# Kernel tuning notes

Measured on AMD Instinct MI355X. Metric: run time of the kernel, lower is better.

The kernel has to match this reference:

```python
import jax, jax.numpy as jnp
import numpy as np
from jax import lax

SCALE = 2
K_UP = 5
EPS = 1e-5
DN = ('NCHW', 'OIHW', 'NCHW')


def _bn(x, gamma, beta, mean, var):
    inv = gamma / jnp.sqrt(var + EPS)
    return x * inv[None, :, None, None] + (beta - mean * inv)[None, :, None, None]


def _pixel_shuffle(x, r):
    b, crr, h, w = x.shape
    c = crr // (r * r)
    x = x.reshape(b, c, r, r, h, w)
    x = x.transpose(0, 1, 4, 2, 5, 3)  # b, c, h, r, w, r
    return x.reshape(b, c, h * r, w * r)


def setup_inputs() -> dict:
    key = jax.random.key(0)
    ks = jax.random.split(key, 4)
    b, c, h, w = 4, 64, 128, 128
    c_mid = 64
    enc_out = (SCALE * K_UP) ** 2  # 100
    return {
        'X': jax.random.normal(ks[0], (b, c, h, w), jnp.float32),
        'comp_w': jax.random.normal(ks[1], (c_mid, c, 1, 1), jnp.float32) * 0.1,
        'comp_gamma': jnp.ones((c_mid,), jnp.float32),
        'comp_beta': jnp.zeros((c_mid,), jnp.float32),
        'comp_mean': jnp.zeros((c_mid,), jnp.float32),
        'comp_var': jnp.ones((c_mid,), jnp.float32),
        'enc_w': jax.random.normal(ks[2], (enc_out, c_mid, 3, 3), jnp.float32) * 0.05,
        'enc_b': jnp.zeros((enc_out,), jnp.float32),
        'enc_gamma': jnp.ones((enc_out,), jnp.float32),
        'enc_beta': jnp.zeros((enc_out,), jnp.float32),
        'enc_mean': jnp.zeros((enc_out,), jnp.float32),
        'enc_var': jnp.ones((enc_out,), jnp.float32),
    }


def reference(X, comp_w, comp_gamma, comp_beta, comp_mean, comp_var,
              enc_w, enc_b, enc_gamma, enc_beta, enc_mean, enc_var):
    b, c, h, w = X.shape
    h_, w_ = h * SCALE, w * SCALE
    # compress: 1x1 conv + BN + ReLU
    Wm = lax.conv_general_dilated(X, comp_w, (1, 1), 'VALID', dimension_numbers=DN)
    Wm = jax.nn.relu(_bn(Wm, comp_gamma, comp_beta, comp_mean, comp_var))
    # encode kernel weights: 3x3 conv + BN
    Wm = lax.conv_general_dilated(Wm, enc_w, (1, 1), ((1, 1), (1, 1)), dimension_numbers=DN)
    Wm = Wm + enc_b[None, :, None, None]
    Wm = _bn(Wm, enc_gamma, enc_beta, enc_mean, enc_var)
    # pixel shuffle -> [b, k_up^2, h_, w_], softmax over kernel dim
    Wm = _pixel_shuffle(Wm, SCALE)
    Wm = jax.nn.softmax(Wm, axis=1)
    # nearest upsample input
    Xu = jnp.repeat(jnp.repeat(X, SCALE, axis=2), SCALE, axis=3)  # [b,c,h_,w_]
    # unfold(k=5, dilation=2, pad=4) + einsum, fused as accumulation over the
    # 25 kernel taps (avoids the b*c*25*h_*w_ im2col blowup; identical math)
    pad = (K_UP // 2) * SCALE  # 4
    Xp = jnp.pad(Xu, ((0, 0), (0, 0), (pad, pad), (pad, pad)))
    out = jnp.zeros((b, c, h_, w_), X.dtype)
    for i in range(K_UP):
        for j in range(K_UP):
            k = i * K_UP + j
            patch = lax.dynamic_slice(Xp, (0, 0, i * SCALE, j * SCALE), (b, c, h_, w_))
            out = out + Wm[:, k:k + 1] * patch
    return out
```

## Files before the change

kernel.cpp:

```cpp
#include <hip/hip_runtime.h>

#define EPS 1e-5f

typedef __attribute__((ext_vector_type(8))) short short8;
typedef __attribute__((ext_vector_type(4))) float float4v;

__device__ inline unsigned short f2bf(float f) {
  unsigned u = __float_as_uint(f);
  unsigned r = (u + 0x7fffu + ((u >> 16) & 1u)) >> 16;
  return (unsigned short)r;
}
__device__ inline uint pk2(float a, float b) {
  return (uint)f2bf(a) | ((uint)f2bf(b) << 16);
}

__global__ __launch_bounds__(256) void xform_kernel(
    const float* __restrict__ enc_w, const float* __restrict__ enc_gamma,
    const float* __restrict__ enc_var, const float* __restrict__ comp_w,
    const float* __restrict__ comp_gamma, const float* __restrict__ comp_var,
    const float* __restrict__ enc_b, const float* __restrict__ enc_beta,
    const float* __restrict__ enc_mean, const float* __restrict__ comp_beta,
    const float* __restrict__ comp_mean, ushort* __restrict__ Awt,
    float* __restrict__ Wc, float* __restrict__ bias2,
    float* __restrict__ bias_c) {
  int u = blockIdx.x * 256 + threadIdx.x;
  if (u < 9216) {
    int kc = u >> 9, rem = u & 511;
    int mt = rem >> 6, q = (rem >> 4) & 3, ml = rem & 15;
    int e = mt * 16 + ml;
    int t = kc >> 1, h = kc & 1;
    int dy = t / 3, dx = t - dy * 3;
    float inv = (e < 100) ? enc_gamma[e] * rsqrtf(enc_var[e] + EPS) : 0.f;
    ushort o[8];
#pragma unroll
    for (int j = 0; j < 8; ++j) {
      int ci = h * 32 + q * 8 + j;
      float w = (e < 100) ? enc_w[(e * 64 + ci) * 9 + dy * 3 + dx] * inv : 0.f;
      o[j] = f2bf(w);
    }
    uint4 v;
    v.x = (uint)o[0] | ((uint)o[1] << 16);
    v.y = (uint)o[2] | ((uint)o[3] << 16);
    v.z = (uint)o[4] | ((uint)o[5] << 16);
    v.w = (uint)o[6] | ((uint)o[7] << 16);
    *reinterpret_cast<uint4*>(Awt + (size_t)u * 8) = v;
  } else if (u < 13312) {
    int v = u - 9216;
    int co = v & 63;
    float inv = comp_gamma[co] * rsqrtf(comp_var[co] + EPS);
    Wc[v] = comp_w[co * 64 + (v >> 6)] * inv;
  } else if (u < 13440) {
    int t = u - 13312;
    float v = 0.f;
    if (t < 100) {
      float inv = enc_gamma[t] * rsqrtf(enc_var[t] + EPS);
      v = enc_b[t] * inv + enc_beta[t] - enc_mean[t] * inv;
    }
    bias2[t] = v;
  } else if (u < 13504) {
    int c = u - 13440;
    float inv = comp_gamma[c] * rsqrtf(comp_var[c] + EPS);
    bias_c[c] = comp_beta[c] - comp_mean[c] * inv;
  }
}

__global__ __launch_bounds__(256) void compress_kernel(
    const float* __restrict__ X, const float* __restrict__ Wc,
    const float* __restrict__ bias_c, ushort* __restrict__ out,
    ushort* __restrict__ Xb) {
  __shared__ __align__(16) float xtile[64 * 65];
  __shared__ __align__(16) float osm[64 * 68];
  const int tid = threadIdx.x;
  const int p0 = blockIdx.x * 64;
  const int b = p0 >> 14;
  const float* xbase = X + ((size_t)b << 20) + (p0 & 16383);

#pragma unroll
  for (int k = 0; k < 16; ++k) {
    int u = k * 256 + tid;
    int ci = u >> 6, px = u & 63;
    xtile[px * 65 + ci] = xbase[((size_t)ci << 14) + px];
  }
  __syncthreads();

  const int wv = __builtin_amdgcn_readfirstlane(tid >> 6);
  const int ln = tid & 63;
  float acc[16];
#pragma unroll
  for (int u = 0; u < 16; ++u) acc[u] = bias_c[wv * 16 + u];
  const float* xr = xtile + ln * 65;
#pragma unroll 8
  for (int ci = 0; ci < 64; ++ci) {
    float xv = xr[ci];
    const float* wr = Wc + ci * 64 + wv * 16;
#pragma unroll
    for (int u = 0; u < 16; ++u) acc[u] = fmaf(wr[u], xv, acc[u]);
  }
  float4v* orow = reinterpret_cast<float4v*>(osm) + ln * 17 + wv * 4;
#pragma unroll
  for (int j = 0; j < 4; ++j) {
    float4v t;
#pragma unroll
    for (int s = 0; s < 4; ++s) t[s] = fmaxf(acc[j * 4 + s], 0.f);
    orow[j] = t;
  }
  __syncthreads();

#pragma unroll
  for (int j = 0; j < 2; ++j) {
    int u = j * 256 + tid;
    int px = u >> 3, g = u & 7;
    const float* so = osm + px * 68 + g * 8;
    uint4 vo = make_uint4(pk2(so[0], so[1]), pk2(so[2], so[3]),
                          pk2(so[4], so[5]), pk2(so[6], so[7]));
    *reinterpret_cast<uint4*>(out + (size_t)(p0 + px) * 64 + g * 8) = vo;
    const float* sx = xtile + px * 65 + g * 8;
    uint4 vx = make_uint4(pk2(sx[0], sx[1]), pk2(sx[2], sx[3]),
                          pk2(sx[4], sx[5]), pk2(sx[6], sx[7]));
    *reinterpret_cast<uint4*>(Xb + (size_t)(p0 + px) * 64 + g * 8) = vx;
  }
}

__global__ __launch_bounds__(256) void encode_mfma(
    const ushort* __restrict__ Wm1t, const ushort* __restrict__ Awt,
    const float* __restrict__ bias2, uint* __restrict__ Wtu) {
  __shared__ __align__(16) char smem[25856];
  ushort* Xt = (ushort*)smem;
  const int tid = threadIdx.x;
  const int b = blockIdx.z;
  const int y0 = blockIdx.y * 8, x0 = blockIdx.x * 8;

  for (int u = tid; u < 800; u += 256) {
    int pos = u >> 3, cg = u & 7;
    int iy = pos / 10, ix = pos - iy * 10;
    int gy = y0 + iy - 1, gx = x0 + ix - 1;
    uint4 v = make_uint4(0, 0, 0, 0);
    if ((unsigned)gy < 128u && (unsigned)gx < 128u)
      v = *reinterpret_cast<const uint4*>(
          Wm1t + ((((size_t)b << 14) + (gy << 7) + gx) << 6) + cg * 8);
    *reinterpret_cast<uint4*>(&Xt[pos * 72 + cg * 8]) = v;
  }
  __syncthreads();

  const int wave = tid >> 6, lane = tid & 63;
  const int q = lane >> 4, px16 = lane & 15;

  float4v acc[2][4];
#pragma unroll
  for (int a = 0; a < 2; ++a)
#pragma unroll
    for (int n = 0; n < 4; ++n) acc[a][n] = (float4v){0.f, 0.f, 0.f, 0.f};

  const short8* Ap = reinterpret_cast<const short8*>(Awt);
#pragma unroll
  for (int kc = 0; kc < 18; ++kc) {
    const int t = kc >> 1, h = kc & 1;
    const int dy = t / 3, dx = t - dy * 3;
    short8 af[2];
#pragma unroll
    for (int a = 0; a < 2; ++a)
      af[a] = Ap[kc * 512 + (wave * 2 + a) * 64 + lane];
    short8 bfr[4];
#pragma unroll
    for (int n = 0; n < 4; ++n) {
      int p = n * 16 + px16;
      int iy = (p >> 3) + dy, ix = (p & 7) + dx;
      bfr[n] = *reinterpret_cast<const short8*>(
          &Xt[(iy * 10 + ix) * 72 + h * 32 + q * 8]);
    }
#pragma unroll
    for (int a = 0; a < 2; ++a)
#pragma unroll
      for (int n = 0; n < 4; ++n)
        acc[a][n] = __builtin_amdgcn_mfma_f32_16x16x32_bf16(
            af[a], bfr[n], acc[a][n], 0, 0, 0);
  }
  __syncthreads();

  float* wsm = (float*)smem;
#pragma unroll
  for (int a = 0; a < 2; ++a) {
    int ebase = (wave * 2 + a) * 16 + q * 4;
    if (ebase < 100) {
#pragma unroll
      for (int n = 0; n < 4; ++n) {
        int p = n * 16 + px16;
        float* dst = wsm + p * 101 + ebase;
        dst[0] = acc[a][n][0];
        dst[1] = acc[a][n][1];
        dst[2] = acc[a][n][2];
        dst[3] = acc[a][n][3];
      }
    }
  }
  __syncthreads();

  {
    const int px = tid & 63, qd = tid >> 6;
    const int rowbase = (qd >> 1) * 28;
    const int half = qd & 1;
    const float* wp = wsm + px * 101 + qd;
    float v[25];
#pragma unroll
    for (int j = 0; j < 25; ++j) v[j] = wp[4 * j] + bias2[4 * j + qd];
    float m = v[0];
#pragma unroll
    for (int j = 1; j < 25; ++j) m = fmaxf(m, v[j]);
    float s = 0.f;
#pragma unroll
    for (int j = 0; j < 25; ++j) { v[j] = __expf(v[j] - m); s += v[j]; }
    float inv = 1.f / s;
    __syncthreads();
    ushort* wpS = (ushort*)smem;
#pragma unroll
    for (int k = 0; k < 25; ++k)
      wpS[(rowbase + k) * 128 + px * 2 + half] = f2bf(v[k] * inv);
  }
  __syncthreads();

  {
    const uint4* src = (const uint4*)smem;
    uint4* dst = reinterpret_cast<uint4*>(
        Wtu + (size_t)((b * 16 + blockIdx.y) * 16 + blockIdx.x) * 3584);
    for (int u = tid; u < 896; u += 256) dst[u] = src[u];
  }
}

__global__ __launch_bounds__(256) void carafe_kernel(
    const ushort* __restrict__ Xb, const uint* __restrict__ Wtu,
    float* __restrict__ out) {
  const int tid = threadIdx.x;
  const int b = blockIdx.z;
  const int y0 = blockIdx.y * 8, x0 = blockIdx.x * 8;
  __shared__ __align__(16) ushort xt[144 * 72];

  for (int u = tid; u < 1152; u += 256) {
    int pos = u >> 3, cg = u & 7;
    int iy = pos / 12, ix = pos - iy * 12;
    int gy = y0 + iy - 2, gx = x0 + ix - 2;
    uint4 v = make_uint4(0, 0, 0, 0);
    if ((unsigned)gy < 128u && (unsigned)gx < 128u)
      v = *reinterpret_cast<const uint4*>(
          Xb + (((size_t)b * 16384 + gy * 128 + gx) << 6) + cg * 8);
    *reinterpret_cast<uint4*>(&xt[pos * 72 + cg * 8]) = v;
  }
  __syncthreads();

  const int p = tid & 63, q = tid >> 6;
  const int r1 = q & 1, cq = q >> 1;
  const int py = p >> 3, px = p & 7;

  const uint* wt = Wtu +
      (size_t)((b * 16 + blockIdx.y) * 16 + blockIdx.x) * 3584 +
      (r1 * 28) * 64 + p;
  uint w[25];
#pragma unroll
  for (int j = 0; j < 25; ++j) w[j] = wt[j * 64];

  float2 acc[32];
#pragma unroll
  for (int i = 0; i < 32; ++i) acc[i] = make_float2(0.f, 0.f);

#pragma unroll
  for (int k = 0; k < 25; ++k) {
    const int dy = k / 5, dx = k - dy * 5;
    const ushort* bp = xt + ((py + dy) * 12 + (px + dx)) * 72 + cq * 32;
    float w0 = __uint_as_float(w[k] << 16);
    float w1 = __uint_as_float(w[k] & 0xffff0000u);
#pragma unroll
    for (int j = 0; j < 4; ++j) {
      uint4 xv = *reinterpret_cast<const uint4*>(bp + 8 * j);
      const uint xu[4] = {xv.x, xv.y, xv.z, xv.w};
#pragma unroll
      for (int t = 0; t < 4; ++t) {
        float xlo = __uint_as_float(xu[t] << 16);
        float xhi = __uint_as_float(xu[t] & 0xffff0000u);
        int c = j * 8 + t * 2;
        acc[c].x = fmaf(w0, xlo, acc[c].x);
        acc[c].y = fmaf(w1, xlo, acc[c].y);
        acc[c + 1].x = fmaf(w0, xhi, acc[c + 1].x);
        acc[c + 1].y = fmaf(w1, xhi, acc[c + 1].y);
      }
    }
  }

  int yq = (y0 + py) * 2 + r1;
  int xq = (x0 + px) * 2;
#pragma unroll
  for (int ci = 0; ci < 32; ++ci) {
    int c = cq * 32 + ci;
    *reinterpret_cast<float2*>(
        out + ((size_t)(b * 64 + c) * 256 + yq) * 256 + xq) = acc[ci];
  }
}

extern "C" void kernel_launch(void* const* d_in, const int* in_sizes, int n_in,
                              void* d_out, int out_size, void* d_ws, size_t ws_size,
                              hipStream_t stream) {
  const float* X          = (const float*)d_in[0];
  const float* comp_w     = (const float*)d_in[1];
  const float* comp_gamma = (const float*)d_in[2];
  const float* comp_beta  = (const float*)d_in[3];
  const float* comp_mean  = (const float*)d_in[4];
  const float* comp_var   = (const float*)d_in[5];
  const float* enc_w      = (const float*)d_in[6];
  const float* enc_b      = (const float*)d_in[7];
  const float* enc_gamma  = (const float*)d_in[8];
  const float* enc_beta   = (const float*)d_in[9];
  const float* enc_mean   = (const float*)d_in[10];
  const float* enc_var    = (const float*)d_in[11];
  float* out = (float*)d_out;

  char* ws = (char*)d_ws;
  ushort* Wm1t  = (ushort*)(ws);
  uint*   Wtu   = (uint*)(ws + 8388608);
  ushort* Xb    = (ushort*)(ws + 23068672);
  ushort* Awt   = (ushort*)(ws + 31457280);
  float*  Wc    = (float*)(ws + 31604736);
  float*  bias2 = (float*)(ws + 31621120);
  float*  biasc = (float*)(ws + 31621632);

  xform_kernel<<<53, 256, 0, stream>>>(enc_w, enc_gamma, enc_var,
                                       comp_w, comp_gamma, comp_var,
                                       enc_b, enc_beta, enc_mean,
                                       comp_beta, comp_mean,
                                       Awt, Wc, bias2, biasc);
  compress_kernel<<<1024, 256, 0, stream>>>(X, Wc, biasc, Wm1t, Xb);
  encode_mfma<<<dim3(16, 16, 4), 256, 0, stream>>>(Wm1t, Awt, bias2, Wtu);
  carafe_kernel<<<dim3(16, 16, 4), 256, 0, stream>>>(Xb, Wtu, out);
}
```

Before: 142.3 us.

## Widen CARAFE tile to 16x8 with 1024 threads and 8-channel-per-thread work split

```diff
diff --git a/kernel.cpp b/kernel.cpp
--- a/kernel.cpp
+++ b/kernel.cpp
@@ -226,17 +226,17 @@
   }
 }
 
-__global__ __launch_bounds__(256) void carafe_kernel(
+__global__ __launch_bounds__(1024, 4) void carafe_kernel(
     const ushort* __restrict__ Xb, const uint* __restrict__ Wtu,
     float* __restrict__ out) {
   const int tid = threadIdx.x;
   const int b = blockIdx.z;
-  const int y0 = blockIdx.y * 8, x0 = blockIdx.x * 8;
-  __shared__ __align__(16) ushort xt[144 * 72];
-
-  for (int u = tid; u < 1152; u += 256) {
+  const int y0 = blockIdx.y * 8, x0 = blockIdx.x * 16;
+  __shared__ __align__(16) ushort xt[240 * 72];
+
+  for (int u = tid; u < 1920; u += 1024) {
     int pos = u >> 3, cg = u & 7;
-    int iy = pos / 12, ix = pos - iy * 12;
+    int iy = pos / 20, ix = pos - iy * 20;
     int gy = y0 + iy - 2, gx = x0 + ix - 2;
     uint4 v = make_uint4(0, 0, 0, 0);
     if ((unsigned)gy < 128u && (unsigned)gx < 128u)
@@ -246,51 +246,56 @@
   }
   __syncthreads();
 
-  const int p = tid & 63, q = tid >> 6;
-  const int r1 = q & 1, cq = q >> 1;
-  const int py = p >> 3, px = p & 7;
-
-  const uint* wt = Wtu +
-      (size_t)((b * 16 + blockIdx.y) * 16 + blockIdx.x) * 3584 +
-      (r1 * 28) * 64 + p;
-  uint w[25];
-#pragma unroll
-  for (int j = 0; j < 25; ++j) w[j] = wt[j * 64];
-
-  float2 acc[32];
-#pragma unroll
-  for (int i = 0; i < 32; ++i) acc[i] = make_float2(0.f, 0.f);
+  const int cg = tid >> 7;
+  const int p = tid & 127;
+  const int yl = p >> 4, xl = p & 15;
+
+  const int tile = (b * 16 + blockIdx.y) * 16 + blockIdx.x * 2 + (xl >> 3);
+  const uint* wt = Wtu + (size_t)tile * 3584 + (yl * 8 + (xl & 7));
+
+  float2 acc0[8], acc1[8];
+#pragma unroll
+  for (int i = 0; i < 8; ++i) {
+    acc0[i] = make_float2(0.f, 0.f);
+    acc1[i] = make_float2(0.f, 0.f);
+  }
 
 #pragma unroll
   for (int k = 0; k < 25; ++k) {
     const int dy = k / 5, dx = k - dy * 5;
-    const ushort* bp = xt + ((py + dy) * 12 + (px + dx)) * 72 + cq * 32;
-    float w0 = __uint_as_float(w[k] << 16);
-    float w1 = __uint_as_float(w[k] & 0xffff0000u);
-#pragma unroll
-    for (int j = 0; j < 4; ++j) {
-      uint4 xv = *reinterpret_cast<const uint4*>(bp + 8 * j);
-      const uint xu[4] = {xv.x, xv.y, xv.z, xv.w};
-#pragma unroll
-      for (int t = 0; t < 4; ++t) {
-        float xlo = __uint_as_float(xu[t] << 16);
-        float xhi = __uint_as_float(xu[t] & 0xffff0000u);
-        int c = j * 8 + t * 2;
-        acc[c].x = fmaf(w0, xlo, acc[c].x);
-        acc[c].y = fmaf(w1, xlo, acc[c].y);
-        acc[c + 1].x = fmaf(w0, xhi, acc[c + 1].x);
-        acc[c + 1].y = fmaf(w1, xhi, acc[c + 1].y);
-      }
-    }
-  }
-
-  int yq = (y0 + py) * 2 + r1;
-  int xq = (x0 + px) * 2;
-#pragma unroll
-  for (int ci = 0; ci < 32; ++ci) {
-    int c = cq * 32 + ci;
-    *reinterpret_cast<float2*>(
-        out + ((size_t)(b * 64 + c) * 256 + yq) * 256 + xq) = acc[ci];
+    const ushort* bp = xt + ((yl + dy) * 20 + (xl + dx)) * 72 + cg * 8;
+    uint wk0 = wt[k * 64];
+    uint wk1 = wt[(28 + k) * 64];
+    float w00 = __uint_as_float(wk0 << 16);
+    float w01 = __uint_as_float(wk0 & 0xffff0000u);
+    float w10 = __uint_as_float(wk1 << 16);
+    float w11 = __uint_as_float(wk1 & 0xffff0000u);
+    uint4 xv = *reinterpret_cast<const uint4*>(bp);
+    const uint xu[4] = {xv.x, xv.y, xv.z, xv.w};
+#pragma unroll
+    for (int t = 0; t < 4; ++t) {
+      float xlo = __uint_as_float(xu[t] << 16);
+      float xhi = __uint_as_float(xu[t] & 0xffff0000u);
+      int c = t * 2;
+      acc0[c].x = fmaf(w00, xlo, acc0[c].x);
+      acc0[c].y = fmaf(w01, xlo, acc0[c].y);
+      acc1[c].x = fmaf(w10, xlo, acc1[c].x);
+      acc1[c].y = fmaf(w11, xlo, acc1[c].y);
+      acc0[c + 1].x = fmaf(w00, xhi, acc0[c + 1].x);
+      acc0[c + 1].y = fmaf(w01, xhi, acc0[c + 1].y);
+      acc1[c + 1].x = fmaf(w10, xhi, acc1[c + 1].x);
+      acc1[c + 1].y = fmaf(w11, xhi, acc1[c + 1].y);
+    }
+  }
+
+  const int yq0 = (y0 + yl) * 2;
+  const int xq = (x0 + xl) * 2;
+#pragma unroll
+  for (int ci = 0; ci < 8; ++ci) {
+    int c = cg * 8 + ci;
+    float* o = out + ((size_t)(b * 64 + c) * 256 + yq0) * 256 + xq;
+    *reinterpret_cast<float2*>(o) = acc0[ci];
+    *reinterpret_cast<float2*>(o + 256) = acc1[ci];
   }
 }
 
@@ -327,5 +332,5 @@
                                        Awt, Wc, bias2, biasc);
   compress_kernel<<<1024, 256, 0, stream>>>(X, Wc, biasc, Wm1t, Xb);
   encode_mfma<<<dim3(16, 16, 4), 256, 0, stream>>>(Wm1t, Awt, bias2, Wtu);
-  carafe_kernel<<<dim3(16, 16, 4), 256, 0, stream>>>(Xb, Wtu, out);
-}
+  carafe_kernel<<<dim3(8, 16, 4), 1024, 0, stream>>>(Xb, Wtu, out);
+}
```

Measured after the change: 161.2 us. 1.13x slower.
